# Optimization experiments

Measured on AMD Instinct MI355X. Metric: run time of the kernel, lower is better.

## Reference

```python
import jax, jax.numpy as jnp
import numpy as np

NH, DK, DV, KC = 12, 64, 128, 4  # heads, head_qk_dim, head_v_dim, conv_size


def causal_dwconv(x, w):
    # x: [B, L, C], w: [C, K] depthwise causal conv (torch Conv1d groups=C with left pad K-1)
    K = w.shape[1]
    L = x.shape[1]
    xp = jnp.pad(x, ((0, 0), (K - 1, 0), (0, 0)))
    out = xp[:, 0:L, :] * w[:, 0]
    for j in range(1, K):
        out = out + xp[:, j:j + L, :] * w[:, j]
    return out


def l2norm(x, eps=1e-12):
    n = jnp.sqrt(jnp.sum(x * x, axis=-1, keepdims=True))
    return x / jnp.maximum(n, eps)


def rmsnorm(x, eps=1e-5):
    return x * jax.lax.rsqrt(jnp.mean(x * x, axis=-1, keepdims=True) + eps)


def setup_inputs() -> dict:
    key = jax.random.key(0)
    ks = jax.random.split(key, 16)
    B, L, H = 4, 2048, 1024
    Kd, Vd = 768, 1536  # key_dim, value_dim
    s = 0.02
    inp = {
        'hidden_states': jax.random.normal(ks[0], (B, L, H), jnp.float32),
        'Wq': jax.random.normal(ks[1], (H, Kd), jnp.float32) * s,
        'Wk': jax.random.normal(ks[2], (H, Kd), jnp.float32) * s,
        'Wv': jax.random.normal(ks[3], (H, Vd), jnp.float32) * s,
        'Wg': jax.random.normal(ks[4], (H, Vd), jnp.float32) * s,
        'Wgk': jax.random.normal(ks[5], (H, NH), jnp.float32) * s,
        'Wb': jax.random.normal(ks[6], (H, NH), jnp.float32) * s,
        'bb': jnp.zeros((NH,), jnp.float32),
        'conv_q': jax.random.normal(ks[7], (Kd, KC), jnp.float32) * 0.3,
        'conv_k': jax.random.normal(ks[8], (Kd, KC), jnp.float32) * 0.3,
        'conv_v': jax.random.normal(ks[9], (Vd, KC), jnp.float32) * 0.3,
        'A_log': jnp.log(jax.random.uniform(ks[10], (NH,), jnp.float32, 1e-4, 16.0)),
        'gnorm_w': jnp.ones((DV,), jnp.float32),
        'Wo': jax.random.normal(ks[11], (Vd, H), jnp.float32) * s,
    }
    dt = jnp.exp(jax.random.uniform(ks[12], (NH,), jnp.float32) * (np.log(0.1) - np.log(0.001)) + np.log(0.001))
    dt = jnp.clip(dt, 1e-4, None)
    inp['dt_bias'] = dt + jnp.log(-jnp.expm1(-dt))
    return inp


def reference(hidden_states, Wq, Wk, Wv, Wg, Wgk, Wb, bb, conv_q, conv_k, conv_v, A_log, dt_bias, gnorm_w, Wo):
    B, L, H = hidden_states.shape
    # projections + causal depthwise short conv with silu (qk_norm='l2')
    q = jax.nn.silu(causal_dwconv(hidden_states @ Wq, conv_q))
    k = jax.nn.silu(causal_dwconv(hidden_states @ Wk, conv_k))
    v = jax.nn.silu(causal_dwconv(hidden_states @ Wv, conv_v))
    # mamba-style decay gate: gk = -exp(A_log) * softplus(x Wgk + dt_bias)  -> [B,L,NH]
    gk = -jnp.exp(A_log) * jax.nn.softplus(hidden_states @ Wgk + dt_bias)
    beta = jax.nn.sigmoid(hidden_states @ Wb + bb)  # [B,L,NH]
    q = l2norm(q.reshape(B, L, NH, DK))
    k = l2norm(k.reshape(B, L, NH, DK))
    v = v.reshape(B, L, NH, DV)

    # gated delta rule recurrence: S_t = exp(gk_t) * S_{t-1}; S_t += k_t (beta_t (v_t - k_t^T S_t)); o_t = q_t^T S_t
    def step(S, inp_t):
        qt, kt, vt, gt, bt = inp_t
        S = S * jnp.exp(gt)[..., None, None]
        pred = jnp.einsum('bhk,bhkv->bhv', kt, S)
        delta = bt[..., None] * (vt - pred)
        S = S + kt[..., None] * delta[:, :, None, :]
        ot = jnp.einsum('bhk,bhkv->bhv', qt, S)
        return S, ot

    xs = (jnp.moveaxis(q, 1, 0), jnp.moveaxis(k, 1, 0), jnp.moveaxis(v, 1, 0),
          jnp.moveaxis(gk, 1, 0), jnp.moveaxis(beta, 1, 0))
    S0 = jnp.zeros((B, NH, DK, DV), hidden_states.dtype)
    _, o = jax.lax.scan(step, S0, xs)
    o = jnp.moveaxis(o, 0, 1)  # [B,L,NH,DV]

    # fused RMSNorm + swish gate, then output projection
    g = (hidden_states @ Wg).reshape(B, L, NH, DV)
    o = rmsnorm(o) * gnorm_w * jax.nn.silu(g)
    return o.reshape(B, L, NH * DV) @ Wo
```

## Files before the change

### kernel.cpp

```cpp
#include <hip/hip_runtime.h>

#define B_   4
#define L_   2048
#define H_   1024
#define KD   768
#define VD   1536
#define NHh  12
#define DKh  64
#define DVh  128
#define M_   (B_ * L_)
#define NC   32
#define NCID (B_ * NHh * NC)

using bf16x8 = __attribute__((ext_vector_type(8))) __bf16;
using f32x4  = __attribute__((ext_vector_type(4))) float;
using ui4    = __attribute__((ext_vector_type(4))) unsigned int;
using f4v    = __attribute__((ext_vector_type(4))) float;
using u16x4  = __attribute__((ext_vector_type(4))) unsigned short;
using u16x8  = __attribute__((ext_vector_type(8))) unsigned short;

__device__ __forceinline__ float bf2f(unsigned short u) {
  unsigned int x = ((unsigned int)u) << 16;
  return __builtin_bit_cast(float, x);
}
__device__ __forceinline__ unsigned short f2bf(float f) {
  unsigned int u = __builtin_bit_cast(unsigned int, f);
  u += 0x7fffu + ((u >> 16) & 1u);
  return (unsigned short)(u >> 16);
}
__device__ __forceinline__ float sigmoidf_(float x) { return 1.f / (1.f + __expf(-x)); }

__device__ __forceinline__ void async_copy16(const unsigned short* __restrict__ g,
                                             unsigned short* l) {
  __builtin_amdgcn_global_load_lds((const __attribute__((address_space(1))) unsigned int*)g,
                                   (__attribute__((address_space(3))) unsigned int*)l, 16, 0, 0);
}

__global__ void detect_dtype(const unsigned short* __restrict__ hs, int* __restrict__ flag) {
  int tid = threadIdx.x;
  int cnt = 0;
  for (int i = tid; i < 1024; i += 256) {
    int e = (hs[i] >> 7) & 0xFF;
    if (e >= 134) cnt++;
  }
  #pragma unroll
  for (int off = 32; off; off >>= 1) cnt += __shfl_xor(cnt, off);
  __shared__ int red[4];
  if ((tid & 63) == 0) red[tid >> 6] = cnt;
  __syncthreads();
  if (tid == 0) *flag = (red[0] + red[1] + red[2] + red[3] > 100) ? 1 : 0;
}

__global__ void convert_hs4(const void* __restrict__ src, unsigned short* __restrict__ dst,
                            const int* __restrict__ flag) {
  size_t i = ((size_t)blockIdx.x * 256 + threadIdx.x) * 4;
  if (*flag) {
    f4v v = *(const f4v*)((const float*)src + i);
    u16x4 o;
    o.x = f2bf(v[0]); o.y = f2bf(v[1]); o.z = f2bf(v[2]); o.w = f2bf(v[3]);
    *(u16x4*)(dst + i) = o;
  } else {
    *(u16x4*)(dst + i) = *(const u16x4*)((const unsigned short*)src + i);
  }
}

__global__ void convert_small(const void* s0, const void* s1, const void* s2,
                              const void* s3, const void* s4, const void* s5, const void* s6,
                              float* d0, float* d1, float* d2, float* d3, float* d4,
                              float* d5, float* d6, const int* __restrict__ flag) {
  const int sizes[7] = {KD * 4, KD * 4, VD * 4, NHh, NHh, NHh, DVh};
  int a = blockIdx.y;
  const void* s; float* d;
  switch (a) {
    case 0: s = s0; d = d0; break;  case 1: s = s1; d = d1; break;
    case 2: s = s2; d = d2; break;  case 3: s = s3; d = d3; break;
    case 4: s = s4; d = d4; break;  case 5: s = s5; d = d5; break;
    default: s = s6; d = d6; break;
  }
  int i = blockIdx.x * 256 + threadIdx.x;
  if (i >= sizes[a]) return;
  float v = (*flag) ? ((const float*)s)[i] : bf2f(((const unsigned short*)s)[i]);
  if (a < 3) {
    int C = (a == 2) ? VD : KD;
    d[(i & 3) * C + (i >> 2)] = v;
  } else {
    d[i] = v;
  }
}

__global__ void transpose_conv(const void* __restrict__ in, unsigned short* __restrict__ out,
                               int R, int C, const int* __restrict__ flag) {
  __shared__ unsigned short tile[32][33];
  int f = *flag;
  int c0 = blockIdx.x * 32, r0 = blockIdx.y * 32;
  int tx = threadIdx.x & 31, ty = threadIdx.x >> 5;
  #pragma unroll
  for (int i = 0; i < 32; i += 8) {
    int r = r0 + ty + i, c = c0 + tx;
    unsigned short v = 0;
    if (r < R && c < C)
      v = f ? f2bf(((const float*)in)[(size_t)r * C + c])
            : ((const unsigned short*)in)[(size_t)r * C + c];
    tile[ty + i][tx] = v;
  }
  __syncthreads();
  #pragma unroll
  for (int i = 0; i < 32; i += 8) {
    int c = c0 + ty + i, r = r0 + tx;
    if (c < C && r < R) out[(size_t)c * R + r] = tile[tx][ty + i];
  }
}

#define BMt 128
#define BNt 128
#define BKt 64

__global__ __launch_bounds__(512, 4) void gemm_bt(
    const unsigned short* __restrict__ Ag,
    const unsigned short* __restrict__ BTg,
    void* __restrict__ Cg,
    int M, int N, int K, int f32mode, const int* __restrict__ flag) {
  __shared__ __align__(16) unsigned short As[2][BMt * BKt];
  __shared__ __align__(16) unsigned short Bs[2][BNt * BKt];
  const int tid = threadIdx.x;
  const int wave = tid >> 6, lane = tid & 63;
  const int wr = wave >> 2, wc = wave & 3;
  const int lrow = lane & 15, lq = lane >> 4;
  const int row0 = blockIdx.x * BMt;
  const int bcol0 = blockIdx.y * BNt;
  unsigned short* Cb = (unsigned short*)Cg;
  int col0 = bcol0, Nst = N;
  if (f32mode == 3) {
    int region = bcol0 / 1536;
    Cb += (size_t)region * (size_t)M_ * 1536;
    col0 = bcol0 - region * 1536;
    Nst = 1536;
  }
  f32x4 acc[4][2] = {};
  auto stage = [&](int sb, int k0) {
    #pragma unroll
    for (int i = 0; i < 2; i++) {
      int c = i * 512 + tid;
      int r = c >> 3;
      int kk = ((c & 7) ^ (r & 7)) << 3;
      int ldsbase = (i * 512 + wave * 64) * 8;
      async_copy16(&Ag[(size_t)(row0 + r) * K + k0 + kk], &As[sb][ldsbase]);
      async_copy16(&BTg[(size_t)(bcol0 + r) * K + k0 + kk], &Bs[sb][ldsbase]);
    }
  };
  const int NT = K / BKt;
  stage(0, 0);
  if (NT > 1) stage(1, BKt);
  for (int t = 0; t < NT; t++) {
    if (t + 1 < NT) asm volatile("s_waitcnt vmcnt(4)" ::: "memory");
    else            asm volatile("s_waitcnt vmcnt(0)" ::: "memory");
    __builtin_amdgcn_s_barrier();
    const int cur = t & 1;
    #pragma unroll
    for (int ks = 0; ks < BKt; ks += 32) {
      bf16x8 af[4], bfr[2];
      #pragma unroll
      for (int i = 0; i < 4; i++) {
        int ra = wr * 64 + i * 16 + lrow;
        int sa = ((ks >> 3) + lq) ^ (ra & 7);
        af[i]  = *(const bf16x8*)&As[cur][ra * BKt + (sa << 3)];
      }
      #pragma unroll
      for (int i = 0; i < 2; i++) {
        int rb = wc * 32 + i * 16 + lrow;
        int sb2 = ((ks >> 3) + lq) ^ (rb & 7);
        bfr[i] = *(const bf16x8*)&Bs[cur][rb * BKt + (sb2 << 3)];
      }
      __builtin_amdgcn_s_setprio(1);
      #pragma unroll
      for (int mi = 0; mi < 4; mi++)
        #pragma unroll
        for (int ni = 0; ni < 2; ni++)
          acc[mi][ni] = __builtin_amdgcn_mfma_f32_16x16x32_bf16(af[mi], bfr[ni], acc[mi][ni], 0, 0, 0);
      __builtin_amdgcn_s_setprio(0);
    }
    __builtin_amdgcn_s_barrier();
    if (t + 2 < NT) stage(cur, (t + 2) * BKt);
  }
  bool f32 = (f32mode == 1) || (f32mode == 2 && *flag != 0);
  #pragma unroll
  for (int mi = 0; mi < 4; mi++)
    #pragma unroll
    for (int ni = 0; ni < 2; ni++)
      #pragma unroll
      for (int r = 0; r < 4; r++) {
        int rr = row0 + wr * 64 + mi * 16 + lq * 4 + r;
        int cc = col0 + wc * 32 + ni * 16 + lrow;
        float v = acc[mi][ni][r];
        if (f32) ((float*)Cg)[(size_t)rr * N + cc] = v;
        else     Cb[(size_t)rr * Nst + cc] = f2bf(v);
      }
}

__global__ void gkbeta_kernel(const float* __restrict__ logits,
                              const float* __restrict__ bb,
                              const float* __restrict__ A_log,
                              const float* __restrict__ dt_bias,
                              float* __restrict__ gkb, float* __restrict__ betab) {
  int idx = blockIdx.x * 256 + threadIdx.x;
  int m = idx / 24, j = idx - m * 24;
  float x = logits[(size_t)m * 128 + j];
  if (j < 12) {
    float t = x + dt_bias[j];
    float sp = (t > 20.f) ? t : log1pf(__expf(t));
    gkb[m * NHh + j] = -__expf(A_log[j]) * sp;
  } else {
    betab[m * NHh + (j - 12)] = sigmoidf_(x + bb[j - 12]);
  }
}

__global__ __launch_bounds__(192) void conv_qk_kernel(
    const unsigned short* __restrict__ raw, int rstride,
    const float* __restrict__ w,
    unsigned short* __restrict__ outp) {
  int tid = threadIdx.x;
  int rib = tid / 96, within = tid - rib * 96;
  int bl = blockIdx.x * 2 + rib;
  int c = within * 8;
  int l = bl & (L_ - 1);
  float acc[8] = {};
  #pragma unroll
  for (int j = 0; j < 4; j++) {
    int ll = l - 3 + j;
    if (ll >= 0) {
      u16x8 v = *(const u16x8*)&raw[(size_t)(bl - 3 + j) * rstride + c];
      f4v w0 = *(const f4v*)&w[j * KD + c];
      f4v w1 = *(const f4v*)&w[j * KD + c + 4];
      #pragma unroll
      for (int e = 0; e < 4; e++) acc[e] += bf2f(v[e]) * w0[e];
      #pragma unroll
      for (int e = 0; e < 4; e++) acc[4 + e] += bf2f(v[4 + e]) * w1[e];
    }
  }
  float x[8], ss = 0.f;
  #pragma unroll
  for (int e = 0; e < 8; e++) {
    float a = acc[e];
    x[e] = a * sigmoidf_(a);
    ss += x[e] * x[e];
  }
  #pragma unroll
  for (int off = 1; off <= 4; off <<= 1) ss += __shfl_xor(ss, off);
  float inv = 1.f / fmaxf(sqrtf(ss), 1e-12f);
  u16x8 o;
  #pragma unroll
  for (int e = 0; e < 8; e++) o[e] = f2bf(x[e] * inv);
  *(u16x8*)&outp[(size_t)bl * KD + c] = o;
}

__global__ void conv_v_kernel(const unsigned short* __restrict__ raw,
                              const float* __restrict__ w,
                              unsigned short* __restrict__ outp) {
  int idx = blockIdx.x * 256 + threadIdx.x;
  int bl = idx / 192;
  int c = (idx - bl * 192) * 8;
  int l = bl & (L_ - 1);
  float acc[8] = {};
  #pragma unroll
  for (int j = 0; j < 4; j++) {
    int ll = l - 3 + j;
    if (ll >= 0) {
      u16x8 v = *(const u16x8*)&raw[(size_t)(bl - 3 + j) * VD + c];
      f4v w0 = *(const f4v*)&w[j * VD + c];
      f4v w1 = *(const f4v*)&w[j * VD + c + 4];
      #pragma unroll
      for (int e = 0; e < 4; e++) acc[e] += bf2f(v[e]) * w0[e];
      #pragma unroll
      for (int e = 0; e < 4; e++) acc[4 + e] += bf2f(v[4 + e]) * w1[e];
    }
  }
  u16x8 o;
  #pragma unroll
  for (int e = 0; e < 8; e++) {
    float a = acc[e];
    o[e] = f2bf(a * sigmoidf_(a));
  }
  *(u16x8*)&outp[(size_t)bl * VD + c] = o;
}

__global__ __launch_bounds__(256) void phase1_kernel(
    const unsigned short* __restrict__ kb, const unsigned short* __restrict__ vb,
    const float* __restrict__ gkb, const float* __restrict__ betab,
    unsigned short* __restrict__ U0g, unsigned short* __restrict__ Wmg,
    float* __restrict__ Gamg) {
  int cid = blockIdx.x;
  int c = cid & (NC - 1), bh = cid >> 5;
  int h = bh % NHh, b = bh / NHh;
  int bl0 = b * L_ + (c << 6);
  __shared__ __align__(16) unsigned short K_lds[64][72];
  __shared__ __align__(16) unsigned short Ab[64][72];
  __shared__ __align__(16) unsigned short Tb[64][72];
  __shared__ __align__(16) unsigned short TbT[64][72];
  __shared__ __align__(16) unsigned short Qt[64][40];
  __shared__ __align__(16) unsigned short Mpad[16][40];
  __shared__ __align__(16) unsigned short RHSt[192][72];
  __shared__ float G_lds[64], beta_lds[64], besc_lds[64];
  int tid = threadIdx.x;
  int wave = tid >> 6, lane = tid & 63, lq = lane >> 4, lrow = lane & 15;
  {
    u16x4 z = {};
    unsigned short* tb = &Tb[0][0];  unsigned short* tt = &TbT[0][0];
    for (int i = tid * 4; i < 64 * 72; i += 1024) {
      *(u16x4*)&tb[i] = z;  *(u16x4*)&tt[i] = z;
    }
    unsigned short* qt = &Qt[0][0];
    for (int i = tid * 4; i < 64 * 40; i += 1024) *(u16x4*)&qt[i] = z;
    if (tid < 160) *(u16x4*)&(&Mpad[0][0])[tid * 4] = z;
  }
  {
    int j = tid >> 2, d0 = (tid & 3) << 4;
    const ui4* src = (const ui4*)&kb[(size_t)(bl0 + j) * KD + h * 64 + d0];
    *(ui4*)&K_lds[j][d0]     = src[0];
    *(ui4*)&K_lds[j][d0 + 8] = src[1];
  }
  if (tid < 64) {
    float g  = gkb[(size_t)(bl0 + tid) * NHh + h];
    float bt = betab[(size_t)(bl0 + tid) * NHh + h];
    #pragma unroll
    for (int off = 1; off < 64; off <<= 1) {
      int src = lane - off;
      float y = __shfl(g, src < 0 ? 0 : src);
      if (lane >= off) g += y;
    }
    G_lds[tid]    = g;
    beta_lds[tid] = bt;
    besc_lds[tid] = bt * __expf(g);
    Gamg[(size_t)cid * 64 + tid] = g;
  }
  __syncthreads();
  #pragma unroll
  for (int mt = 0; mt < 4; mt++) {
    f32x4 acc = {};
    #pragma unroll
    for (int ks = 0; ks < 2; ks++) {
      bf16x8 a  = *(const bf16x8*)&K_lds[wave * 16 + lrow][ks * 32 + lq * 8];
      bf16x8 b2 = *(const bf16x8*)&K_lds[mt * 16 + lrow][ks * 32 + lq * 8];
      acc = __builtin_amdgcn_mfma_f32_16x16x32_bf16(a, b2, acc, 0, 0, 0);
    }
    #pragma unroll
    for (int r = 0; r < 4; r++) {
      int j = wave * 16 + lq * 4 + r, m = mt * 16 + lrow;
      Ab[j][m] = (m < j) ? f2bf(beta_lds[j] * __expf(G_lds[j] - G_lds[m]) * acc[r])
                         : (unsigned short)0;
    }
  }
  __syncthreads();
  if (wave == 0) {
    int blk = lq, cc = lrow, base = blk * 16;
    float t[16];
    t[0] = (cc == 0) ? 1.f : 0.f;
    #pragma unroll
    for (int j = 1; j < 16; j++) {
      float s = 0.f;
      #pragma unroll
      for (int m = 0; m < j; m++)
        s += bf2f(Ab[base + j][base + m]) * t[m];
      t[j] = ((cc == j) ? 1.f : 0.f) - s;
    }
    #pragma unroll
    for (int j = 0; j < 16; j++) {
      unsigned short bv = f2bf(t[j]);
      Tb[base + j][base + cc]  = bv;
      TbT[base + cc][base + j] = bv;
    }
  } else {
    int r = tid - 64;
    if (r < 128) {
      const unsigned short* vp = &vb[(size_t)bl0 * VD + h * 128 + r];
      for (int j = 0; j < 64; j++)
        RHSt[r][j] = f2bf(beta_lds[j] * bf2f(vp[(size_t)j * VD]));
    } else {
      int d = r - 128;
      for (int j = 0; j < 64; j++)
        RHSt[r][j] = f2bf(besc_lds[j] * bf2f(K_lds[j][d]));
    }
  }
  __syncthreads();
  #pragma unroll
  for (int lvl = 1; lvl < 4; lvl++) {
    {
      int m = tid >> 4, k = tid & 15;
      Ab[lvl * 16 + m][lvl * 16 + k] = 0;
      Mpad[m][k] = Tb[lvl * 16 + m][lvl * 16 + k];
    }
    __syncthreads();
    f32x4 accP = {};
    #pragma unroll
    for (int ks2 = 0; ks2 < 2; ks2++) {
      bf16x8 a  = *(const bf16x8*)&Ab[lvl * 16 + lrow][ks2 * 32 + lq * 8];
      bf16x8 b2 = *(const bf16x8*)&TbT[wave * 16 + lrow][ks2 * 32 + lq * 8];
      accP = __builtin_amdgcn_mfma_f32_16x16x32_bf16(a, b2, accP, 0, 0, 0);
    }
    {
      int col = wave * 16 + lrow;
      u16x4 qp;
      #pragma unroll
      for (int r = 0; r < 4; r++) {
        int krow = lq * 4 + r;
        float e = (col == lvl * 16 + krow) ? 1.f : 0.f;
        ((unsigned short*)&qp)[r] = f2bf(e - accP[r]);
      }
      *(u16x4*)&Qt[col][lq * 4] = qp;
    }
    __syncthreads();
    {
      bf16x8 am = *(const bf16x8*)&Mpad[lrow][lq * 8];
      bf16x8 bq = *(const bf16x8*)&Qt[wave * 16 + lrow][lq * 8];
      f32x4 accR = {};
      accR = __builtin_amdgcn_mfma_f32_16x16x32_bf16(am, bq, accR, 0, 0, 0);
      #pragma unroll
      for (int r = 0; r < 4; r++) {
        int row = lvl * 16 + lq * 4 + r, col = wave * 16 + lrow;
        unsigned short bv = f2bf(accR[r]);
        Tb[row][col]  = bv;
        TbT[col][row] = bv;
      }
    }
    __syncthreads();
  }
  bf16x8 af0 = *(const bf16x8*)&Tb[wave * 16 + lrow][lq * 8];
  bf16x8 af1 = *(const bf16x8*)&Tb[wave * 16 + lrow][32 + lq * 8];
  #pragma unroll
  for (int nt = 0; nt < 12; nt++) {
    f32x4 acc = {};
    bf16x8 b0 = *(const bf16x8*)&RHSt[nt * 16 + lrow][lq * 8];
    bf16x8 b1 = *(const bf16x8*)&RHSt[nt * 16 + lrow][32 + lq * 8];
    acc = __builtin_amdgcn_mfma_f32_16x16x32_bf16(af0, b0, acc, 0, 0, 0);
    acc = __builtin_amdgcn_mfma_f32_16x16x32_bf16(af1, b1, acc, 0, 0, 0);
    #pragma unroll
    for (int r = 0; r < 4; r++) {
      int i = wave * 16 + lq * 4 + r;
      int col = nt * 16 + lrow;
      if (nt < 8) U0g[(size_t)cid * 8192 + i * 128 + col] = f2bf(acc[r]);
      else        Wmg[(size_t)cid * 4096 + i * 64 + (col - 128)] = f2bf(acc[r]);
    }
  }
}

__global__ __launch_bounds__(256) void phase2_kernel(
    const unsigned short* __restrict__ kb,
    const unsigned short* __restrict__ U0g, const unsigned short* __restrict__ Wmg,
    const float* __restrict__ Gamg, unsigned short* __restrict__ P0g) {
  int blk = blockIdx.x;
  int vc = blk & 3, bh = blk >> 2;
  int h = bh % NHh, b = bh / NHh;
  __shared__ __align__(16) unsigned short P_bf[32][72];
  __shared__ __align__(16) unsigned short Wm_lds[64][72];
  __shared__ __align__(16) unsigned short Ktmp[64][72];
  __shared__ __align__(16) unsigned short KpT_lds[64][72];
  __shared__ __align__(16) unsigned short U0_lds[64][40];
  __shared__ __align__(16) unsigned short UT_lds[32][72];
  __shared__ float G2[64];
  int tid = threadIdx.x;
  int wave = tid >> 6, lane = tid & 63, lq = lane >> 4, lrow = lane & 15;
  int vt = wave & 1, dbase = (wave >> 1) * 2;
  f32x4 P[2] = {};
  int pj = tid >> 2, px = (tid & 3) << 4;
  int pv = (tid & 3) << 3;
  ui4 pf_wm0, pf_wm1, pf_k0, pf_k1, pf_u0;
  float pf_g = 0.f;
  {
    size_t cid0 = (size_t)bh * NC;
    int bl0 = b * L_;
    pf_wm0 = *(const ui4*)&Wmg[cid0 * 4096 + pj * 64 + px];
    pf_wm1 = *(const ui4*)&Wmg[cid0 * 4096 + pj * 64 + px + 8];
    pf_k0  = *(const ui4*)&kb[(size_t)(bl0 + pj) * KD + h * 64 + px];
    pf_k1  = *(const ui4*)&kb[(size_t)(bl0 + pj) * KD + h * 64 + px + 8];
    pf_u0  = *(const ui4*)&U0g[cid0 * 8192 + pj * 128 + vc * 32 + pv];
    if (tid < 64) pf_g = Gamg[cid0 * 64 + tid];
  }
  for (int c = 0; c < NC; c++) {
    size_t cid = (size_t)bh * NC + c;
    #pragma unroll
    for (int di = 0; di < 2; di++)
      #pragma unroll
      for (int r = 0; r < 4; r++)
        P_bf[vt * 16 + lq * 4 + r][(dbase + di) * 16 + lrow] = f2bf(P[di][r]);
    *(ui4*)&Wm_lds[pj][px]     = pf_wm0;
    *(ui4*)&Wm_lds[pj][px + 8] = pf_wm1;
    *(ui4*)&Ktmp[pj][px]       = pf_k0;
    *(ui4*)&Ktmp[pj][px + 8]   = pf_k1;
    *(ui4*)&U0_lds[pj][pv]     = pf_u0;
    if (tid < 64) G2[tid] = pf_g;
    __syncthreads();
    float gend = __expf(G2[63]);
    {
      int v = tid >> 3, d8 = (tid & 7) << 3;
      *(ui4*)&P0g[cid * 8192 + (size_t)(vc * 32 + v) * 64 + d8] = *(const ui4*)&P_bf[v][d8];
    }
    if (c + 1 < NC) {
      size_t cid1 = cid + 1;
      int bl1 = b * L_ + ((c + 1) << 6);
      pf_wm0 = *(const ui4*)&Wmg[cid1 * 4096 + pj * 64 + px];
      pf_wm1 = *(const ui4*)&Wmg[cid1 * 4096 + pj * 64 + px + 8];
      pf_k0  = *(const ui4*)&kb[(size_t)(bl1 + pj) * KD + h * 64 + px];
      pf_k1  = *(const ui4*)&kb[(size_t)(bl1 + pj) * KD + h * 64 + px + 8];
      pf_u0  = *(const ui4*)&U0g[cid1 * 8192 + pj * 128 + vc * 32 + pv];
      if (tid < 64) pf_g = Gamg[cid1 * 64 + tid];
    }
    {
      int d = tid & 63, j0 = (tid >> 6) << 4;
      float Ge = G2[63];
      #pragma unroll
      for (int i = 0; i < 16; i++) {
        int j = j0 + i;
        KpT_lds[d][j] = f2bf(__expf(Ge - G2[j]) * bf2f(Ktmp[j][d]));
      }
    }
    #pragma unroll
    for (int vt2 = 0; vt2 < 2; vt2++) {
      f32x4 acc = {};
      #pragma unroll
      for (int ks2 = 0; ks2 < 2; ks2++) {
        bf16x8 a  = *(const bf16x8*)&Wm_lds[wave * 16 + lrow][ks2 * 32 + lq * 8];
        bf16x8 b2 = *(const bf16x8*)&P_bf[vt2 * 16 + lrow][ks2 * 32 + lq * 8];
        acc = __builtin_amdgcn_mfma_f32_16x16x32_bf16(a, b2, acc, 0, 0, 0);
      }
      u16x4 p;
      #pragma unroll
      for (int r = 0; r < 4; r++) {
        int j = wave * 16 + lq * 4 + r;
        ((unsigned short*)&p)[r] = f2bf(bf2f(U0_lds[j][vt2 * 16 + lrow]) - acc[r]);
      }
      *(u16x4*)&UT_lds[vt2 * 16 + lrow][wave * 16 + lq * 4] = p;
    }
    __syncthreads();
    #pragma unroll
    for (int di = 0; di < 2; di++) {
      f32x4 acc = P[di];
      #pragma unroll
      for (int r = 0; r < 4; r++) acc[r] *= gend;
      #pragma unroll
      for (int ks2 = 0; ks2 < 2; ks2++) {
        bf16x8 a  = *(const bf16x8*)&UT_lds[vt * 16 + lrow][ks2 * 32 + lq * 8];
        bf16x8 b2 = *(const bf16x8*)&KpT_lds[(dbase + di) * 16 + lrow][ks2 * 32 + lq * 8];
        acc = __builtin_amdgcn_mfma_f32_16x16x32_bf16(a, b2, acc, 0, 0, 0);
      }
      P[di] = acc;
    }
  }
}

__global__ __launch_bounds__(256) void phase3_kernel(
    const unsigned short* __restrict__ qb, const unsigned short* __restrict__ kb,
    const unsigned short* __restrict__ U0g, const unsigned short* __restrict__ Wmg,
    const unsigned short* __restrict__ P0g, const float* __restrict__ Gamg,
    unsigned short* __restrict__ o_raw) {
  int cid = blockIdx.x;
  int c = cid & (NC - 1), bh = cid >> 5;
  int h = bh % NHh, b = bh / NHh;
  int bl0 = b * L_ + (c << 6);
  __shared__ __align__(16) unsigned short Q_lds[64][72];
  __shared__ __align__(16) unsigned short K_lds[64][72];
  __shared__ __align__(16) unsigned short WM_lds[64][72];
  __shared__ __align__(16) unsigned short P0_lds[128][72];
  __shared__ __align__(16) unsigned short U0_lds[64][128];
  __shared__ __align__(16) unsigned short UT_lds[128][72];
  __shared__ float G_lds[64];
  int tid = threadIdx.x;
  int wave = tid >> 6, lane = tid & 63, lq = lane >> 4, lrow = lane & 15;
  {
    int j = tid >> 2, d0 = (tid & 3) << 4;
    const ui4* qs = (const ui4*)&qb[(size_t)(bl0 + j) * KD + h * 64 + d0];
    *(ui4*)&Q_lds[j][d0] = qs[0];  *(ui4*)&Q_lds[j][d0 + 8] = qs[1];
    const ui4* ks = (const ui4*)&kb[(size_t)(bl0 + j) * KD + h * 64 + d0];
    *(ui4*)&K_lds[j][d0] = ks[0];  *(ui4*)&K_lds[j][d0 + 8] = ks[1];
    const ui4* ws = (const ui4*)&Wmg[(size_t)cid * 4096 + j * 64 + d0];
    *(ui4*)&WM_lds[j][d0] = ws[0]; *(ui4*)&WM_lds[j][d0 + 8] = ws[1];
    int v = tid >> 1, e0 = (tid & 1) << 5;
    const ui4* ps = (const ui4*)&P0g[(size_t)cid * 8192 + v * 64 + e0];
    *(ui4*)&P0_lds[v][e0]      = ps[0]; *(ui4*)&P0_lds[v][e0 + 8]  = ps[1];
    *(ui4*)&P0_lds[v][e0 + 16] = ps[2]; *(ui4*)&P0_lds[v][e0 + 24] = ps[3];
    int e1 = tid * 32;
    const ui4* us = (const ui4*)&U0g[(size_t)cid * 8192 + e1];
    ui4* ud = (ui4*)&U0_lds[0][e1];
    ud[0] = us[0]; ud[1] = us[1]; ud[2] = us[2]; ud[3] = us[3];
    if (tid < 64) G_lds[tid] = Gamg[(size_t)cid * 64 + tid];
  }
  __syncthreads();
  #pragma unroll
  for (int nt = 0; nt < 8; nt++) {
    f32x4 acc = {};
    #pragma unroll
    for (int ks2 = 0; ks2 < 2; ks2++) {
      bf16x8 a  = *(const bf16x8*)&WM_lds[wave * 16 + lrow][ks2 * 32 + lq * 8];
      bf16x8 b2 = *(const bf16x8*)&P0_lds[nt * 16 + lrow][ks2 * 32 + lq * 8];
      acc = __builtin_amdgcn_mfma_f32_16x16x32_bf16(a, b2, acc, 0, 0, 0);
    }
    u16x4 p;
    #pragma unroll
    for (int r = 0; r < 4; r++) {
      int j = wave * 16 + lq * 4 + r;
      ((unsigned short*)&p)[r] = f2bf(bf2f(U0_lds[j][nt * 16 + lrow]) - acc[r]);
    }
    *(u16x4*)&UT_lds[nt * 16 + lrow][wave * 16 + lq * 4] = p;
  }
  __syncthreads();
  #pragma unroll
  for (int mt = 0; mt < 4; mt++) {
    f32x4 acc = {};
    #pragma unroll
    for (int ks2 = 0; ks2 < 2; ks2++) {
      bf16x8 a  = *(const bf16x8*)&Q_lds[wave * 16 + lrow][ks2 * 32 + lq * 8];
      bf16x8 b2 = *(const bf16x8*)&K_lds[mt * 16 + lrow][ks2 * 32 + lq * 8];
      acc = __builtin_amdgcn_mfma_f32_16x16x32_bf16(a, b2, acc, 0, 0, 0);
    }
    #pragma unroll
    for (int r = 0; r < 4; r++) {
      int i = wave * 16 + lq * 4 + r, j = mt * 16 + lrow;
      WM_lds[i][j] = (j <= i) ? f2bf(__expf(G_lds[i] - G_lds[j]) * acc[r]) : (unsigned short)0;
    }
  }
  __syncthreads();
  #pragma unroll
  for (int nt = 0; nt < 8; nt++) {
    f32x4 accO = {}, accS = {};
    #pragma unroll
    for (int ks2 = 0; ks2 < 2; ks2++) {
      bf16x8 aM = *(const bf16x8*)&WM_lds[wave * 16 + lrow][ks2 * 32 + lq * 8];
      bf16x8 bU = *(const bf16x8*)&UT_lds[nt * 16 + lrow][ks2 * 32 + lq * 8];
      accO = __builtin_amdgcn_mfma_f32_16x16x32_bf16(aM, bU, accO, 0, 0, 0);
      bf16x8 aQ = *(const bf16x8*)&Q_lds[wave * 16 + lrow][ks2 * 32 + lq * 8];
      bf16x8 bP = *(const bf16x8*)&P0_lds[nt * 16 + lrow][ks2 * 32 + lq * 8];
      accS = __builtin_amdgcn_mfma_f32_16x16x32_bf16(aQ, bP, accS, 0, 0, 0);
    }
    #pragma unroll
    for (int r = 0; r < 4; r++) {
      int i = wave * 16 + lq * 4 + r;
      float o = accO[r] + __expf(G_lds[i]) * accS[r];
      o_raw[(size_t)(bl0 + i) * VD + h * 128 + nt * 16 + lrow] = f2bf(o);
    }
  }
}

__global__ void norm_gate_kernel(unsigned short* __restrict__ o_raw,
                                 const unsigned short* __restrict__ g,
                                 const float* __restrict__ gnw) {
  int tid = threadIdx.x;
  int r = blockIdx.x * 16 + (tid >> 4);
  int v = (tid & 15) * 8;
  u16x8 xo = *(const u16x8*)&o_raw[(size_t)r * DVh + v];
  u16x8 xg = *(const u16x8*)&g[(size_t)r * DVh + v];
  float x[8], ss = 0.f;
  #pragma unroll
  for (int e = 0; e < 8; e++) {
    x[e] = bf2f(xo[e]);
    ss += x[e] * x[e];
  }
  #pragma unroll
  for (int off = 1; off <= 8; off <<= 1) ss += __shfl_xor(ss, off);
  float inv = rsqrtf(ss * (1.f / (float)DVh) + 1e-5f);
  f4v w0 = *(const f4v*)&gnw[v];
  f4v w1 = *(const f4v*)&gnw[v + 4];
  u16x8 o;
  #pragma unroll
  for (int e = 0; e < 8; e++) {
    float gv = bf2f(xg[e]);
    float wv = (e < 4) ? w0[e] : w1[e - 4];
    o[e] = f2bf(x[e] * inv * wv * (gv * sigmoidf_(gv)));
  }
  *(u16x8*)&o_raw[(size_t)r * DVh + v] = o;
}

extern "C" void kernel_launch(void* const* d_in, const int* in_sizes, int n_in,
                              void* d_out, int out_size, void* d_ws, size_t ws_size,
                              hipStream_t stream) {
  const void* hs      = d_in[0];
  const void* Wq      = d_in[1];
  const void* Wk      = d_in[2];
  const void* Wv      = d_in[3];
  const void* Wg      = d_in[4];
  const void* Wgk     = d_in[5];
  const void* Wb      = d_in[6];
  const void* bb      = d_in[7];
  const void* cq      = d_in[8];
  const void* ck      = d_in[9];
  const void* cv      = d_in[10];
  const void* A_log   = d_in[11];
  const void* gnorm_w = d_in[12];
  const void* Wo      = d_in[13];
  const void* dt_bias = d_in[14];

  char* wsB = (char*)d_ws;
  size_t off = 0;
  auto walloc = [&](size_t bytes) -> char* {
    char* p = wsB + off;
    off += (bytes + 1023) & ~(size_t)1023;
    return p;
  };
  int* flag = (int*)walloc(1024);
  unsigned short* WqT   = (unsigned short*)walloc((size_t)KD * H_ * 2);
  unsigned short* WkT   = (unsigned short*)walloc((size_t)KD * H_ * 2);
  unsigned short* WvT   = (unsigned short*)walloc((size_t)VD * H_ * 2);
  unsigned short* WgT   = (unsigned short*)walloc((size_t)VD * H_ * 2);
  unsigned short* WgkbT = (unsigned short*)walloc((size_t)128 * H_ * 2);
  unsigned short* WoT   = (unsigned short*)walloc((size_t)H_ * VD * 2);
  float* cqf   = (float*)walloc((size_t)KD * 4 * 4);
  float* ckf   = (float*)walloc((size_t)KD * 4 * 4);
  float* cvf   = (float*)walloc((size_t)VD * 4 * 4);
  float* bbf   = (float*)walloc(NHh * 4);
  float* A_logf= (float*)walloc(NHh * 4);
  float* dtf   = (float*)walloc(NHh * 4);
  float* gnwf  = (float*)walloc(DVh * 4);
  float* gkb   = (float*)walloc((size_t)M_ * NHh * 4);
  float* betab = (float*)walloc((size_t)M_ * NHh * 4);
  float* Gamg  = (float*)walloc((size_t)NCID * 64 * 4);
  unsigned short* c_hs  = (unsigned short*)walloc((size_t)M_ * H_ * 2);
  unsigned short* qkraw = (unsigned short*)walloc((size_t)M_ * 1536 * 2);
  unsigned short* vraw  = (unsigned short*)walloc((size_t)M_ * VD * 2);
  unsigned short* gbuf  = (unsigned short*)walloc((size_t)M_ * VD * 2);
  unsigned short* qb    = (unsigned short*)walloc((size_t)M_ * KD * 2);
  unsigned short* kb    = (unsigned short*)walloc((size_t)M_ * KD * 2);
  unsigned short* vb    = (unsigned short*)walloc((size_t)M_ * VD * 2);
  float*          logits32 = (float*)vraw;
  unsigned short* Wmg   = c_hs;
  unsigned short* U0g   = qkraw;
  unsigned short* o_raw = vraw;
  unsigned short* P0g   = vb;

  detect_dtype<<<1, 256, 0, stream>>>((const unsigned short*)hs, flag);
  convert_small<<<dim3(24, 7), 256, 0, stream>>>(cq, ck, cv, bb, A_log, dt_bias, gnorm_w,
                                                 cqf, ckf, cvf, bbf, A_logf, dtf, gnwf, flag);
  transpose_conv<<<dim3(KD / 32, H_ / 32), 256, 0, stream>>>(Wq, WqT, H_, KD, flag);
  transpose_conv<<<dim3(KD / 32, H_ / 32), 256, 0, stream>>>(Wk, WkT, H_, KD, flag);
  transpose_conv<<<dim3(VD / 32, H_ / 32), 256, 0, stream>>>(Wv, WvT, H_, VD, flag);
  transpose_conv<<<dim3(VD / 32, H_ / 32), 256, 0, stream>>>(Wg, WgT, H_, VD, flag);
  transpose_conv<<<dim3(1, H_ / 32), 256, 0, stream>>>(Wgk, WgkbT, H_, NHh, flag);
  transpose_conv<<<dim3(1, H_ / 32), 256, 0, stream>>>(Wb, WgkbT + 12 * H_, H_, NHh, flag);
  transpose_conv<<<dim3(H_ / 32, VD / 32), 256, 0, stream>>>(Wo, WoT, VD, H_, flag);
  convert_hs4<<<(M_ * H_) / 1024, 256, 0, stream>>>(hs, c_hs, flag);

  gemm_bt<<<dim3(M_ / 128, 1), 512, 0, stream>>>(c_hs, WgkbT, logits32, M_, 128, H_, 1, flag);
  gkbeta_kernel<<<(M_ * 24) / 256, 256, 0, stream>>>(logits32, bbf, A_logf, dtf, gkb, betab);
  gemm_bt<<<dim3(M_ / 128, 4608 / 128), 512, 0, stream>>>(c_hs, WqT, qkraw, M_, 4608, H_, 3, flag);

  conv_qk_kernel<<<M_ / 2, 192, 0, stream>>>(qkraw, 1536, cqf, qb);
  conv_qk_kernel<<<M_ / 2, 192, 0, stream>>>(qkraw + KD, 1536, ckf, kb);
  conv_v_kernel<<<(M_ * 192) / 256, 256, 0, stream>>>(vraw, cvf, vb);

  phase1_kernel<<<NCID, 256, 0, stream>>>(kb, vb, gkb, betab, U0g, Wmg, Gamg);
  phase2_kernel<<<B_ * NHh * 4, 256, 0, stream>>>(kb, U0g, Wmg, Gamg, P0g);
  phase3_kernel<<<NCID, 256, 0, stream>>>(qb, kb, U0g, Wmg, P0g, Gamg, o_raw);

  norm_gate_kernel<<<(M_ * NHh) / 16, 256, 0, stream>>>(o_raw, gbuf, gnwf);

  gemm_bt<<<dim3(M_ / 128, H_ / 128), 512, 0, stream>>>(o_raw, WoT, d_out, M_, H_, VD, 2, flag);
}
```

Measured before the change: 446.2 us.

## Fuse gk/beta activation into GEMM epilogue and norm-gate into phase3

The gk/beta logits GEMM now applies softplus/sigmoid in its epilogue and writes gkb/betab directly, which removes the separate gkbeta kernel and the fp32 logits round trip. The RMSNorm and swish gating are folded into phase3. It prefetches the gate tile into registers, stashes it in reused LDS, computes row sum-of-squares with shuffles and writes the final gated output. This drops a kernel launch and a full read-write pass over o_raw, at the cost of more register pressure in phase3.

```diff
diff --git a/kernel.cpp b/kernel.cpp
--- a/kernel.cpp
+++ b/kernel.cpp
@@ -119,7 +119,10 @@
     const unsigned short* __restrict__ Ag,
     const unsigned short* __restrict__ BTg,
     void* __restrict__ Cg,
-    int M, int N, int K, int f32mode, const int* __restrict__ flag) {
+    int M, int N, int K, int f32mode, const int* __restrict__ flag,
+    const float* __restrict__ bbf, const float* __restrict__ A_logf,
+    const float* __restrict__ dtf,
+    float* __restrict__ gkb, float* __restrict__ betab) {
   __shared__ __align__(16) unsigned short As[2][BMt * BKt];
   __shared__ __align__(16) unsigned short Bs[2][BNt * BKt];
   const int tid = threadIdx.x;
@@ -182,6 +185,26 @@
     __builtin_amdgcn_s_barrier();
     if (t + 2 < NT) stage(cur, (t + 2) * BKt);
   }
+  if (f32mode == 4) {
+    #pragma unroll
+    for (int mi = 0; mi < 4; mi++)
+      #pragma unroll
+      for (int ni = 0; ni < 2; ni++)
+        #pragma unroll
+        for (int r = 0; r < 4; r++) {
+          int rr = row0 + wr * 64 + mi * 16 + lq * 4 + r;
+          int cc = wc * 32 + ni * 16 + lrow;
+          float v = acc[mi][ni][r];
+          if (cc < 12) {
+            float tt = v + dtf[cc];
+            float sp = (tt > 20.f) ? tt : log1pf(__expf(tt));
+            gkb[(size_t)rr * NHh + cc] = -__expf(A_logf[cc]) * sp;
+          } else if (cc < 24) {
+            betab[(size_t)rr * NHh + (cc - 12)] = sigmoidf_(v + bbf[cc - 12]);
+          }
+        }
+    return;
+  }
   bool f32 = (f32mode == 1) || (f32mode == 2 && *flag != 0);
   #pragma unroll
   for (int mi = 0; mi < 4; mi++)
@@ -195,23 +218,6 @@
         if (f32) ((float*)Cg)[(size_t)rr * N + cc] = v;
         else     Cb[(size_t)rr * Nst + cc] = f2bf(v);
       }
-}
-
-__global__ void gkbeta_kernel(const float* __restrict__ logits,
-                              const float* __restrict__ bb,
-                              const float* __restrict__ A_log,
-                              const float* __restrict__ dt_bias,
-                              float* __restrict__ gkb, float* __restrict__ betab) {
-  int idx = blockIdx.x * 256 + threadIdx.x;
-  int m = idx / 24, j = idx - m * 24;
-  float x = logits[(size_t)m * 128 + j];
-  if (j < 12) {
-    float t = x + dt_bias[j];
-    float sp = (t > 20.f) ? t : log1pf(__expf(t));
-    gkb[m * NHh + j] = -__expf(A_log[j]) * sp;
-  } else {
-    betab[m * NHh + (j - 12)] = sigmoidf_(x + bb[j - 12]);
-  }
 }
 
 __global__ __launch_bounds__(192) void conv_qk_kernel(
@@ -550,6 +556,7 @@
     const unsigned short* __restrict__ qb, const unsigned short* __restrict__ kb,
     const unsigned short* __restrict__ U0g, const unsigned short* __restrict__ Wmg,
     const unsigned short* __restrict__ P0g, const float* __restrict__ Gamg,
+    const unsigned short* __restrict__ gb, const float* __restrict__ gnw,
     unsigned short* __restrict__ o_raw) {
   int cid = blockIdx.x;
   int c = cid & (NC - 1), bh = cid >> 5;
@@ -564,6 +571,15 @@
   __shared__ float G_lds[64];
   int tid = threadIdx.x;
   int wave = tid >> 6, lane = tid & 63, lq = lane >> 4, lrow = lane & 15;
+  ui4 gpre[4];
+  float gnww[8];
+  {
+    int j = tid >> 2, c0 = (tid & 3) << 5;
+    const ui4* gs = (const ui4*)&gb[(size_t)(bl0 + j) * VD + h * 128 + c0];
+    gpre[0] = gs[0]; gpre[1] = gs[1]; gpre[2] = gs[2]; gpre[3] = gs[3];
+    #pragma unroll
+    for (int nt = 0; nt < 8; nt++) gnww[nt] = gnw[nt * 16 + lrow];
+  }
   {
     int j = tid >> 2, d0 = (tid & 3) << 4;
     const ui4* qs = (const ui4*)&qb[(size_t)(bl0 + j) * KD + h * 64 + d0];
@@ -601,6 +617,11 @@
     *(u16x4*)&UT_lds[nt * 16 + lrow][wave * 16 + lq * 4] = p;
   }
   __syncthreads();
+  {
+    int j = tid >> 2, c0 = (tid & 3) << 5;
+    ui4* gd = (ui4*)&U0_lds[j][c0];
+    gd[0] = gpre[0]; gd[1] = gpre[1]; gd[2] = gpre[2]; gd[3] = gpre[3];
+  }
   #pragma unroll
   for (int mt = 0; mt < 4; mt++) {
     f32x4 acc = {};
@@ -617,6 +638,10 @@
     }
   }
   __syncthreads();
+  float ov[8][4];
+  float eg[4];
+  #pragma unroll
+  for (int r = 0; r < 4; r++) eg[r] = __expf(G_lds[wave * 16 + lq * 4 + r]);
   #pragma unroll
   for (int nt = 0; nt < 8; nt++) {
     f32x4 accO = {}, accS = {};
@@ -630,41 +655,28 @@
       accS = __builtin_amdgcn_mfma_f32_16x16x32_bf16(aQ, bP, accS, 0, 0, 0);
     }
     #pragma unroll
+    for (int r = 0; r < 4; r++) ov[nt][r] = accO[r] + eg[r] * accS[r];
+  }
+  float inv_[4];
+  #pragma unroll
+  for (int r = 0; r < 4; r++) {
+    float ss = 0.f;
+    #pragma unroll
+    for (int nt = 0; nt < 8; nt++) ss += ov[nt][r] * ov[nt][r];
+    #pragma unroll
+    for (int off2 = 1; off2 <= 8; off2 <<= 1) ss += __shfl_xor(ss, off2);
+    inv_[r] = rsqrtf(ss * (1.f / 128.f) + 1e-5f);
+  }
+  #pragma unroll
+  for (int nt = 0; nt < 8; nt++) {
+    #pragma unroll
     for (int r = 0; r < 4; r++) {
       int i = wave * 16 + lq * 4 + r;
-      float o = accO[r] + __expf(G_lds[i]) * accS[r];
+      float gv = bf2f(U0_lds[i][nt * 16 + lrow]);
+      float o = ov[nt][r] * inv_[r] * gnww[nt] * (gv * sigmoidf_(gv));
       o_raw[(size_t)(bl0 + i) * VD + h * 128 + nt * 16 + lrow] = f2bf(o);
     }
   }
-}
-
-__global__ void norm_gate_kernel(unsigned short* __restrict__ o_raw,
-                                 const unsigned short* __restrict__ g,
-                                 const float* __restrict__ gnw) {
-  int tid = threadIdx.x;
-  int r = blockIdx.x * 16 + (tid >> 4);
-  int v = (tid & 15) * 8;
-  u16x8 xo = *(const u16x8*)&o_raw[(size_t)r * DVh + v];
-  u16x8 xg = *(const u16x8*)&g[(size_t)r * DVh + v];
-  float x[8], ss = 0.f;
-  #pragma unroll
-  for (int e = 0; e < 8; e++) {
-    x[e] = bf2f(xo[e]);
-    ss += x[e] * x[e];
-  }
-  #pragma unroll
-  for (int off = 1; off <= 8; off <<= 1) ss += __shfl_xor(ss, off);
-  float inv = rsqrtf(ss * (1.f / (float)DVh) + 1e-5f);
-  f4v w0 = *(const f4v*)&gnw[v];
-  f4v w1 = *(const f4v*)&gnw[v + 4];
-  u16x8 o;
-  #pragma unroll
-  for (int e = 0; e < 8; e++) {
-    float gv = bf2f(xg[e]);
-    float wv = (e < 4) ? w0[e] : w1[e - 4];
-    o[e] = f2bf(x[e] * inv * wv * (gv * sigmoidf_(gv)));
-  }
-  *(u16x8*)&o_raw[(size_t)r * DVh + v] = o;
 }
 
 extern "C" void kernel_launch(void* const* d_in, const int* in_sizes, int n_in,
@@ -717,7 +729,6 @@
   unsigned short* qb    = (unsigned short*)walloc((size_t)M_ * KD * 2);
   unsigned short* kb    = (unsigned short*)walloc((size_t)M_ * KD * 2);
   unsigned short* vb    = (unsigned short*)walloc((size_t)M_ * VD * 2);
-  float*          logits32 = (float*)vraw;
   unsigned short* Wmg   = c_hs;
   unsigned short* U0g   = qkraw;
   unsigned short* o_raw = vraw;
@@ -735,9 +746,10 @@
   transpose_conv<<<dim3(H_ / 32, VD / 32), 256, 0, stream>>>(Wo, WoT, VD, H_, flag);
   convert_hs4<<<(M_ * H_) / 1024, 256, 0, stream>>>(hs, c_hs, flag);
 
-  gemm_bt<<<dim3(M_ / 128, 1), 512, 0, stream>>>(c_hs, WgkbT, logits32, M_, 128, H_, 1, flag);
-  gkbeta_kernel<<<(M_ * 24) / 256, 256, 0, stream>>>(logits32, bbf, A_logf, dtf, gkb, betab);
-  gemm_bt<<<dim3(M_ / 128, 4608 / 128), 512, 0, stream>>>(c_hs, WqT, qkraw, M_, 4608, H_, 3, flag);
+  gemm_bt<<<dim3(M_ / 128, 1), 512, 0, stream>>>(c_hs, WgkbT, nullptr, M_, 128, H_, 4, flag,
+                                                 bbf, A_logf, dtf, gkb, betab);
+  gemm_bt<<<dim3(M_ / 128, 4608 / 128), 512, 0, stream>>>(c_hs, WqT, qkraw, M_, 4608, H_, 3, flag,
+                                                          nullptr, nullptr, nullptr, nullptr, nullptr);
 
   conv_qk_kernel<<<M_ / 2, 192, 0, stream>>>(qkraw, 1536, cqf, qb);
   conv_qk_kernel<<<M_ / 2, 192, 0, stream>>>(qkraw + KD, 1536, ckf, kb);
@@ -745,9 +757,8 @@
 
   phase1_kernel<<<NCID, 256, 0, stream>>>(kb, vb, gkb, betab, U0g, Wmg, Gamg);
   phase2_kernel<<<B_ * NHh * 4, 256, 0, stream>>>(kb, U0g, Wmg, Gamg, P0g);
-  phase3_kernel<<<NCID, 256, 0, stream>>>(qb, kb, U0g, Wmg, P0g, Gamg, o_raw);
-
-  norm_gate_kernel<<<(M_ * NHh) / 16, 256, 0, stream>>>(o_raw, gbuf, gnwf);
-
-  gemm_bt<<<dim3(M_ / 128, H_ / 128), 512, 0, stream>>>(o_raw, WoT, d_out, M_, H_, VD, 2, flag);
-}
+  phase3_kernel<<<NCID, 256, 0, stream>>>(qb, kb, U0g, Wmg, P0g, Gamg, gbuf, gnwf, o_raw);
+
+  gemm_bt<<<dim3(M_ / 128, H_ / 128), 512, 0, stream>>>(o_raw, WoT, d_out, M_, H_, VD, 2, flag,
+                                                        nullptr, nullptr, nullptr, nullptr, nullptr);
+}
```

Result: no change. 447.8 us (+0.3%).
